# Kernel optimization log

Hardware: AMD Instinct MI355X
Metric: run time of the kernel (lower is better)

Reference implementation:

```python
import jax, jax.numpy as jnp
import numpy as np

N_NODES = 50000
N_EDGES = 800000
D = 128  # hidden_dim == node feature dim


def setup_inputs() -> dict:
    key = jax.random.key(0)
    k1, k2, k3, k4 = jax.random.split(key, 4)
    node_feat = jax.random.normal(k1, (N_NODES, D), dtype=jnp.float32)
    edge_index = jax.random.randint(k2, (2, N_EDGES), 0, N_NODES, dtype=jnp.int32)
    # MLP params: LazyLinear(2D -> D), Linear(D -> D)
    W1 = jax.random.normal(k3, (2 * D, D), dtype=jnp.float32) * (1.0 / np.sqrt(2 * D))
    b1 = jnp.zeros((D,), dtype=jnp.float32)
    W2 = jax.random.normal(k4, (D, D), dtype=jnp.float32) * (1.0 / np.sqrt(D))
    b2 = jnp.zeros((D,), dtype=jnp.float32)
    return {"node_feat": node_feat, "edge_index": edge_index,
            "W1": W1, "b1": b1, "W2": W2, "b2": b2}


def reference(node_feat, edge_index, W1, b1, W2, b2):
    # node_feat: [N, D]; edge_index: [2, E]
    src, dst = edge_index[0], edge_index[1]
    n = node_feat.shape[0]
    # gather source feats [E, D], scatter-add into dst -> [N, D]
    msgs = node_feat[src]
    agg = jax.ops.segment_sum(msgs, dst, num_segments=n)
    # degree normalization (clamp min 1)
    deg = jax.ops.segment_sum(jnp.ones_like(dst, dtype=node_feat.dtype), dst,
                              num_segments=n)
    agg = agg / jnp.maximum(deg, 1.0)[:, None]
    # update MLP on concat([node_feat, agg]); dropout is identity at eval
    h = jnp.concatenate([node_feat, agg], axis=-1)          # [N, 2D]
    h = jax.nn.relu(h @ W1 + b1)                             # [N, D]
    h = jax.nn.relu(h @ W2 + b2)                             # [N, D]
    return h
```

## Files before the change

### kernel.cpp

```cpp
#include <hip/hip_runtime.h>
#include <hip/hip_bf16.h>

#define N_NODES 50000
#define N_EDGES 800000
#define D 128
#define SLOTS 64
#define NTILES 782

typedef __attribute__((ext_vector_type(8))) short short8v;
typedef __attribute__((ext_vector_type(4))) float f32x4;


__device__ __forceinline__ unsigned short f32_to_bf16_rn(float f) {
    unsigned int u = __float_as_uint(f);
    unsigned int r = (u + 0x7fffu + ((u >> 16) & 1u)) >> 16;
    return (unsigned short)r;
}
__device__ __forceinline__ unsigned int pack2(float a, float b) {
    return (unsigned int)f32_to_bf16_rn(a) |
           ((unsigned int)f32_to_bf16_rn(b) << 16);
}
__device__ __forceinline__ float bflo(unsigned int w) {
    return __uint_as_float(w << 16);
}
__device__ __forceinline__ float bfhi(unsigned int w) {
    return __uint_as_float(w & 0xffff0000u);
}

__global__ __launch_bounds__(256) void fill_kernel(
    const int* __restrict__ ei, const float* __restrict__ W1,
    const float* __restrict__ W2, int* __restrict__ cnt,
    unsigned short* __restrict__ ss, unsigned short* __restrict__ Wt1,
    unsigned short* __restrict__ Wt2) {
    int tid = blockIdx.x * 256 + threadIdx.x;
    if (tid < N_EDGES) {
        int dst = ei[N_EDGES + tid];
        int pos = atomicAdd(&cnt[dst], 1);
        if (pos < SLOTS)
            __builtin_nontemporal_store((unsigned short)ei[tid],
                                        &ss[(size_t)dst * SLOTS + pos]);
    }
    int t2 = tid - N_EDGES;
    if (t2 >= 0 && t2 < 128 * 256) {
        int n = t2 >> 8, k = t2 & 255;
        Wt1[t2] = f32_to_bf16_rn(W1[k * 128 + n]);
    }
    int t3 = t2 - 128 * 256;
    if (t3 >= 0 && t3 < 128 * 128) {
        int n = t3 >> 7, k = t3 & 127;
        Wt2[t3] = f32_to_bf16_rn(W2[k * 128 + n]);
    }
}

__global__ __launch_bounds__(256) void prep_kernel(
    const float* __restrict__ x, unsigned short* __restrict__ xb) {
    const int XBW = N_NODES * D / 8;
    int tid = blockIdx.x * 256 + threadIdx.x;
    if (tid >= XBW) return;
    const float4* p = reinterpret_cast<const float4*>(x + (size_t)tid * 8);
    float4 v0 = p[0], v1 = p[1];
    uint4 o;
    o.x = pack2(v0.x, v0.y);
    o.y = pack2(v0.z, v0.w);
    o.z = pack2(v1.x, v1.y);
    o.w = pack2(v1.z, v1.w);
    *reinterpret_cast<uint4*>(xb + (size_t)tid * 8) = o;
}

__global__ __launch_bounds__(256) void aggregate_kernel(
    const unsigned short* __restrict__ xb, const int* __restrict__ cnt,
    const unsigned short* __restrict__ ss, unsigned short* __restrict__ ab) {
    const int lane = threadIdx.x & 63;
    const int row = blockIdx.x * 4 + (threadIdx.x >> 6);
    int dg = cnt[row];
    if (dg > SLOTS) dg = SLOTS;
    const unsigned short* sp = ss + (size_t)row * SLOTS;
    float fx = 0.0f, fy = 0.0f;
    int j = 0;
    for (; j + 8 <= dg; j += 8) {
        int s0 = sp[j + 0];
        int s1 = sp[j + 1];
        int s2 = sp[j + 2];
        int s3 = sp[j + 3];
        int s4 = sp[j + 4];
        int s5 = sp[j + 5];
        int s6 = sp[j + 6];
        int s7 = sp[j + 7];
        unsigned int g0 = reinterpret_cast<const unsigned int*>(xb + (size_t)s0 * D)[lane];
        unsigned int g1 = reinterpret_cast<const unsigned int*>(xb + (size_t)s1 * D)[lane];
        unsigned int g2 = reinterpret_cast<const unsigned int*>(xb + (size_t)s2 * D)[lane];
        unsigned int g3 = reinterpret_cast<const unsigned int*>(xb + (size_t)s3 * D)[lane];
        unsigned int g4 = reinterpret_cast<const unsigned int*>(xb + (size_t)s4 * D)[lane];
        unsigned int g5 = reinterpret_cast<const unsigned int*>(xb + (size_t)s5 * D)[lane];
        unsigned int g6 = reinterpret_cast<const unsigned int*>(xb + (size_t)s6 * D)[lane];
        unsigned int g7 = reinterpret_cast<const unsigned int*>(xb + (size_t)s7 * D)[lane];
        fx += bflo(g0) + bflo(g1) + bflo(g2) + bflo(g3) + bflo(g4) + bflo(g5) +
              bflo(g6) + bflo(g7);
        fy += bfhi(g0) + bfhi(g1) + bfhi(g2) + bfhi(g3) + bfhi(g4) + bfhi(g5) +
              bfhi(g6) + bfhi(g7);
    }
    for (; j + 4 <= dg; j += 4) {
        int s0 = sp[j + 0];
        int s1 = sp[j + 1];
        int s2 = sp[j + 2];
        int s3 = sp[j + 3];
        unsigned int g0 = reinterpret_cast<const unsigned int*>(xb + (size_t)s0 * D)[lane];
        unsigned int g1 = reinterpret_cast<const unsigned int*>(xb + (size_t)s1 * D)[lane];
        unsigned int g2 = reinterpret_cast<const unsigned int*>(xb + (size_t)s2 * D)[lane];
        unsigned int g3 = reinterpret_cast<const unsigned int*>(xb + (size_t)s3 * D)[lane];
        fx += bflo(g0) + bflo(g1) + bflo(g2) + bflo(g3);
        fy += bfhi(g0) + bfhi(g1) + bfhi(g2) + bfhi(g3);
    }
    for (; j < dg; ++j) {
        int s0 = sp[j];
        unsigned int g0 = reinterpret_cast<const unsigned int*>(xb + (size_t)s0 * D)[lane];
        fx += bflo(g0);
        fy += bfhi(g0);
    }
    const float inv = 1.0f / fmaxf((float)dg, 1.0f);
    reinterpret_cast<unsigned int*>(ab + (size_t)row * D)[lane] =
        pack2(fx * inv, fy * inv);
}

__global__ __launch_bounds__(256, 1) void mlp_kernel(
    const unsigned short* __restrict__ xb, const unsigned short* __restrict__ ab,
    const unsigned short* __restrict__ Wt1,
    const unsigned short* __restrict__ Wt2, const float* __restrict__ b1,
    const float* __restrict__ b2, float* __restrict__ out) {
    __shared__ unsigned char w1s[65536];
    __shared__ unsigned char w2s[32768];
    __shared__ unsigned char h1t[4][4096];

    const int tid = threadIdx.x;
    for (int i = tid; i < 4096; i += 256) {
        unsigned o = (unsigned)i * 16;
        uint4 v = reinterpret_cast<const uint4*>(Wt1)[i];
        *reinterpret_cast<uint4*>(w1s + (o ^ (((o >> 9) & 7u) << 4))) = v;
    }
    for (int i = tid; i < 2048; i += 256) {
        unsigned o = (unsigned)i * 16;
        uint4 v = reinterpret_cast<const uint4*>(Wt2)[i];
        *reinterpret_cast<uint4*>(w2s + (o ^ (((o >> 8) & 7u) << 4))) = v;
    }

    const int lane = tid & 63;
    const int wv = tid >> 6;
    const int rloc = lane & 15;
    const int kseg = lane >> 4;
    const unsigned rswz = (unsigned)((rloc & 7) << 4);
    unsigned char* my = h1t[wv];

    float bias1[8], bias2[8];
#pragma unroll
    for (int ct = 0; ct < 8; ++ct) {
        bias1[ct] = b1[ct * 16 + rloc];
        bias2[ct] = b2[ct * 16 + rloc];
    }
    __syncthreads();

    for (int tile = blockIdx.x; tile < NTILES; tile += gridDim.x) {
        const int rbase = tile * 64 + wv * 16;
        int arow = rbase + rloc;
        if (arow >= N_NODES) arow = N_NODES - 1;

        short8v a[8];
#pragma unroll
        for (int kk = 0; kk < 8; ++kk) {
            const unsigned short* ap =
                (kk < 4) ? xb + (size_t)arow * D + kk * 32 + kseg * 8
                         : ab + (size_t)arow * D + (kk - 4) * 32 + kseg * 8;
            a[kk] = *reinterpret_cast<const short8v*>(ap);
        }
        f32x4 acc[8];
#pragma unroll
        for (int ct = 0; ct < 8; ++ct) acc[ct] = (f32x4){0.f, 0.f, 0.f, 0.f};
#pragma unroll
        for (int kk = 0; kk < 8; ++kk) {
#pragma unroll
            for (int ct = 0; ct < 8; ++ct) {
                unsigned off = (unsigned)((ct * 16 + rloc) * 512 + kk * 64 + kseg * 16);
                short8v b = *reinterpret_cast<const short8v*>(w1s + (off ^ rswz));
                acc[ct] = __builtin_amdgcn_mfma_f32_16x16x32_bf16(a[kk], b, acc[ct], 0, 0, 0);
            }
        }
#pragma unroll
        for (int ct = 0; ct < 8; ++ct) {
#pragma unroll
            for (int r = 0; r < 4; ++r) {
                int lrow = kseg * 4 + r;
                float v = fmaxf(acc[ct][r] + bias1[ct], 0.0f);
                unsigned off = (unsigned)(lrow * 256 + (ct * 16 + rloc) * 2);
                *reinterpret_cast<unsigned short*>(
                    my + (off ^ ((unsigned)((lrow & 7) << 4)))) = f32_to_bf16_rn(v);
            }
        }
        __syncthreads();

        short8v a2[4];
#pragma unroll
        for (int kk = 0; kk < 4; ++kk) {
            unsigned off = (unsigned)(rloc * 256 + kk * 64 + kseg * 16);
            a2[kk] = *reinterpret_cast<const short8v*>(my + (off ^ rswz));
        }
        f32x4 acc2[8];
#pragma unroll
        for (int ct = 0; ct < 8; ++ct) acc2[ct] = (f32x4){0.f, 0.f, 0.f, 0.f};
#pragma unroll
        for (int kk = 0; kk < 4; ++kk) {
#pragma unroll
            for (int ct = 0; ct < 8; ++ct) {
                unsigned off = (unsigned)((ct * 16 + rloc) * 256 + kk * 64 + kseg * 16);
                short8v b = *reinterpret_cast<const short8v*>(w2s + (off ^ rswz));
                acc2[ct] = __builtin_amdgcn_mfma_f32_16x16x32_bf16(a2[kk], b, acc2[ct], 0, 0, 0);
            }
        }
        const int orow0 = rbase + kseg * 4;
#pragma unroll
        for (int ct = 0; ct < 8; ++ct) {
#pragma unroll
            for (int r = 0; r < 4; ++r) {
                int row = orow0 + r;
                if (row < N_NODES) {
                    out[(size_t)row * 128 + ct * 16 + rloc] =
                        fmaxf(acc2[ct][r] + bias2[ct], 0.0f);
                }
            }
        }
        __syncthreads();
    }
}

extern "C" void kernel_launch(void* const* d_in, const int* in_sizes, int n_in,
                              void* d_out, int out_size, void* d_ws,
                              size_t ws_size, hipStream_t stream) {
    const float* node_feat = (const float*)d_in[0];
    const int* ei = (const int*)d_in[1];
    const float* W1 = (const float*)d_in[2];
    const float* b1 = (const float*)d_in[3];
    const float* W2 = (const float*)d_in[4];
    const float* b2 = (const float*)d_in[5];
    float* out = (float*)d_out;

    int* cnt = (int*)d_ws;
    unsigned short* ss = (unsigned short*)(cnt + N_NODES);
    unsigned short* xb = ss + (size_t)N_NODES * SLOTS;
    unsigned short* ab = xb + (size_t)N_NODES * D;
    unsigned short* Wt1 = ab + (size_t)N_NODES * D;
    unsigned short* Wt2 = Wt1 + 128 * 256;

    const int fill_threads = N_EDGES + 128 * 256 + 128 * 128;

    hipMemsetAsync(cnt, 0, N_NODES * sizeof(int), stream);
    fill_kernel<<<(fill_threads + 255) / 256, 256, 0, stream>>>(
        ei, W1, W2, cnt, ss, Wt1, Wt2);
    prep_kernel<<<(N_NODES * D / 8 + 255) / 256, 256, 0, stream>>>(node_feat, xb);
    aggregate_kernel<<<N_NODES / 4, 256, 0, stream>>>(xb, cnt, ss, ab);
    mlp_kernel<<<256, 256, 0, stream>>>(xb, ab, Wt1, Wt2, b1, b2, out);
}
```

Before: 126.9 us.

## Bucket edges by destination range before slot scatter for locality

Replaces the single atomic-scatter fill with two passes. The first pass partitions edges into 8 destination-range buckets using shared-memory staging. The second pass scatters each bucket into per-node slot lists, so atomics and slot writes hit a smaller, cache-resident region of the count and slot arrays. The weight transposition moves into the feature-conversion kernel. This adds a kernel launch and an extra round trip of packed edge pairs through global memory. It relies on fixed bucket capacities and on the 16-bit source packing that was already in place.

```diff
diff --git a/kernel.cpp b/kernel.cpp
--- a/kernel.cpp
+++ b/kernel.cpp
@@ -6,6 +6,11 @@
 #define D 128
 #define SLOTS 64
 #define NTILES 782
+#define NBKT 8
+#define BKT_ROWS 6250
+#define BCHUNK 2048
+#define LCAP 384
+#define SCAP 106496
 
 typedef __attribute__((ext_vector_type(8))) short short8v;
 typedef __attribute__((ext_vector_type(4))) float f32x4;
@@ -27,20 +32,85 @@
     return __uint_as_float(w & 0xffff0000u);
 }
 
-__global__ __launch_bounds__(256) void fill_kernel(
-    const int* __restrict__ ei, const float* __restrict__ W1,
-    const float* __restrict__ W2, int* __restrict__ cnt,
-    unsigned short* __restrict__ ss, unsigned short* __restrict__ Wt1,
-    unsigned short* __restrict__ Wt2) {
-    int tid = blockIdx.x * 256 + threadIdx.x;
-    if (tid < N_EDGES) {
-        int dst = ei[N_EDGES + tid];
+__global__ __launch_bounds__(256) void bucket_kernel(
+    const int* __restrict__ ei, int* __restrict__ scnt,
+    unsigned int* __restrict__ pairs) {
+    __shared__ int lcnt[NBKT];
+    __shared__ int lbase[NBKT];
+    __shared__ unsigned int lbuf[NBKT][LCAP];
+    const int tid = threadIdx.x;
+    if (tid < NBKT) lcnt[tid] = 0;
+    __syncthreads();
+    const int e0 = blockIdx.x * BCHUNK;
+#pragma unroll
+    for (int k = 0; k < BCHUNK / 256; ++k) {
+        int e = e0 + k * 256 + tid;
+        if (e < N_EDGES) {
+            int src = ei[e];
+            int dst = ei[N_EDGES + e];
+            int b = dst / BKT_ROWS;
+            unsigned int pk =
+                ((unsigned int)(dst - b * BKT_ROWS) << 16) | (unsigned int)src;
+            int pos = atomicAdd(&lcnt[b], 1);
+            if (pos < LCAP) {
+                lbuf[b][pos] = pk;
+            } else {
+                int gp = atomicAdd(&scnt[b * 32], 1);
+                if (gp < SCAP) pairs[(size_t)b * SCAP + gp] = pk;
+            }
+        }
+    }
+    __syncthreads();
+    if (tid < NBKT) {
+        int c = lcnt[tid];
+        if (c > LCAP) c = LCAP;
+        lcnt[tid] = c;
+        lbase[tid] = atomicAdd(&scnt[tid * 32], c);
+    }
+    __syncthreads();
+    for (int b = 0; b < NBKT; ++b) {
+        const int c = lcnt[b];
+        const int base = lbase[b];
+        for (int i = tid; i < c; i += 256)
+            pairs[(size_t)b * SCAP + base + i] = lbuf[b][i];
+    }
+}
+
+__global__ __launch_bounds__(256) void scatter_kernel(
+    const unsigned int* __restrict__ pairs, const int* __restrict__ scnt,
+    int* __restrict__ cnt, unsigned short* __restrict__ ss) {
+    const int b = blockIdx.x & 7;
+    const int sub = blockIdx.x >> 3;
+    int count = scnt[b * 32];
+    if (count > SCAP) count = SCAP;
+    const unsigned int* sp = pairs + (size_t)b * SCAP;
+    const int rowbase = b * BKT_ROWS;
+    for (int i = sub * 256 + threadIdx.x; i < count; i += 128 * 256) {
+        unsigned int p = sp[i];
+        int dst = rowbase + (int)(p >> 16);
         int pos = atomicAdd(&cnt[dst], 1);
         if (pos < SLOTS)
-            __builtin_nontemporal_store((unsigned short)ei[tid],
-                                        &ss[(size_t)dst * SLOTS + pos]);
-    }
-    int t2 = tid - N_EDGES;
+            ss[(size_t)dst * SLOTS + pos] = (unsigned short)(p & 0xffffu);
+    }
+}
+
+__global__ __launch_bounds__(256) void prep_kernel(
+    const float* __restrict__ x, const float* __restrict__ W1,
+    const float* __restrict__ W2, unsigned short* __restrict__ xb,
+    unsigned short* __restrict__ Wt1, unsigned short* __restrict__ Wt2) {
+    const int XBW = N_NODES * D / 8;
+    int tid = blockIdx.x * 256 + threadIdx.x;
+    if (tid < XBW) {
+        const float4* p = reinterpret_cast<const float4*>(x + (size_t)tid * 8);
+        float4 v0 = p[0], v1 = p[1];
+        uint4 o;
+        o.x = pack2(v0.x, v0.y);
+        o.y = pack2(v0.z, v0.w);
+        o.z = pack2(v1.x, v1.y);
+        o.w = pack2(v1.z, v1.w);
+        *reinterpret_cast<uint4*>(xb + (size_t)tid * 8) = o;
+    }
+    int t2 = tid - XBW;
     if (t2 >= 0 && t2 < 128 * 256) {
         int n = t2 >> 8, k = t2 & 255;
         Wt1[t2] = f32_to_bf16_rn(W1[k * 128 + n]);
@@ -50,21 +120,6 @@
         int n = t3 >> 7, k = t3 & 127;
         Wt2[t3] = f32_to_bf16_rn(W2[k * 128 + n]);
     }
-}
-
-__global__ __launch_bounds__(256) void prep_kernel(
-    const float* __restrict__ x, unsigned short* __restrict__ xb) {
-    const int XBW = N_NODES * D / 8;
-    int tid = blockIdx.x * 256 + threadIdx.x;
-    if (tid >= XBW) return;
-    const float4* p = reinterpret_cast<const float4*>(x + (size_t)tid * 8);
-    float4 v0 = p[0], v1 = p[1];
-    uint4 o;
-    o.x = pack2(v0.x, v0.y);
-    o.y = pack2(v0.z, v0.w);
-    o.z = pack2(v1.x, v1.y);
-    o.w = pack2(v1.z, v1.w);
-    *reinterpret_cast<uint4*>(xb + (size_t)tid * 8) = o;
 }
 
 __global__ __launch_bounds__(256) void aggregate_kernel(
@@ -242,18 +297,23 @@
     float* out = (float*)d_out;
 
     int* cnt = (int*)d_ws;
-    unsigned short* ss = (unsigned short*)(cnt + N_NODES);
+    int* scnt = cnt + N_NODES;
+    unsigned int* pairs = (unsigned int*)(scnt + 256);
+    unsigned short* ss = (unsigned short*)(pairs + (size_t)NBKT * SCAP);
     unsigned short* xb = ss + (size_t)N_NODES * SLOTS;
     unsigned short* ab = xb + (size_t)N_NODES * D;
     unsigned short* Wt1 = ab + (size_t)N_NODES * D;
     unsigned short* Wt2 = Wt1 + 128 * 256;
 
-    const int fill_threads = N_EDGES + 128 * 256 + 128 * 128;
-
-    hipMemsetAsync(cnt, 0, N_NODES * sizeof(int), stream);
-    fill_kernel<<<(fill_threads + 255) / 256, 256, 0, stream>>>(
-        ei, W1, W2, cnt, ss, Wt1, Wt2);
-    prep_kernel<<<(N_NODES * D / 8 + 255) / 256, 256, 0, stream>>>(node_feat, xb);
+    const int XBW = N_NODES * D / 8;
+    const int prep_threads = XBW + 128 * 256 + 128 * 128;
+
+    hipMemsetAsync(cnt, 0, (N_NODES + 256) * sizeof(int), stream);
+    bucket_kernel<<<(N_EDGES + BCHUNK - 1) / BCHUNK, 256, 0, stream>>>(
+        ei, scnt, pairs);
+    scatter_kernel<<<1024, 256, 0, stream>>>(pairs, scnt, cnt, ss);
+    prep_kernel<<<(prep_threads + 255) / 256, 256, 0, stream>>>(
+        node_feat, W1, W2, xb, Wt1, Wt2);
     aggregate_kernel<<<N_NODES / 4, 256, 0, stream>>>(xb, cnt, ss, ab);
     mlp_kernel<<<256, 256, 0, stream>>>(xb, ab, Wt1, Wt2, b1, b2, out);
 }
```

New measurement: 125.0 us. Within noise of the previous version (-1.5%).
